# Performance work log

Hardware: AMD Instinct MI355X
Metric: run time of the kernel (lower is better)

The kernel has to match this reference:

```python
import jax, jax.numpy as jnp
import numpy as np

B, N, U, D, E = 4, 20000, 64, 1, 640000
F = U + D  # node feature dim fed to TransformerConv (state || inputs)
SCALE = 1.0 / float(np.sqrt(U))
NEG = -1e30


def setup_inputs() -> dict:
    key = jax.random.key(0)
    ks = jax.random.split(key, 20)

    def glorot(k, shape):
        s = float(np.sqrt(2.0 / (shape[0] + shape[1])))
        return jax.random.normal(k, shape, jnp.float32) * s

    inp = {
        'inputs': jax.random.normal(ks[0], (B, N), jnp.float32),
        'state': jax.random.normal(ks[1], (B, N * U), jnp.float32),
        'edge_src': jax.random.randint(ks[2], (E,), 0, N),
        'edge_dst': jax.random.randint(ks[3], (E,), 0, N),
        # TransformerConv(U+D -> U, heads=1, concat=False): query/key/value/skip linears
        'Wq': glorot(ks[4], (F, U)), 'bq': jnp.zeros((U,), jnp.float32),
        'Wk': glorot(ks[5], (F, U)), 'bk': jnp.zeros((U,), jnp.float32),
        'Wv': glorot(ks[6], (F, U)), 'bv': jnp.zeros((U,), jnp.float32),
        'Ws': glorot(ks[7], (F, U)), 'bs': jnp.zeros((U,), jnp.float32),
        # GRULinear 1: (U + D) -> 2U ; GRULinear 2: (U + D) -> U
        'W1': glorot(ks[8], (U + D, 2 * U)), 'b1': jnp.zeros((2 * U,), jnp.float32),
        'W2': glorot(ks[9], (U + D, U)), 'b2': jnp.zeros((U,), jnp.float32),
    }
    return inp


def _transformer_conv_masked(x, src, dst, Wq, bq, Wk, bk, Wv, bv, Ws, bs):
    """x: (B, N, F). PyG TransformerConv heads=1 concat=False with node/edge
    masking as in remove_nodes_and_edges (keep nodes with x[:, -7] != 0)."""
    node_mask = x[..., -7] != 0  # (B, N)
    emask = (node_mask[:, src] & node_mask[:, dst]).astype(x.dtype)  # (B, E)

    q = x @ Wq + bq  # (B, N, U)
    k = x @ Wk + bk
    v = x @ Wv + bv

    scores = jnp.einsum('beu,beu->be', q[:, dst], k[:, src]) * SCALE  # (B, E)
    scores_m = jnp.where(emask > 0, scores, NEG)
    m = jnp.full((x.shape[0], N), NEG, x.dtype).at[:, dst].max(scores_m)  # (B, N)
    e = jnp.exp(jnp.where(emask > 0, scores - m[:, dst], 0.0)) * emask  # (B, E)

    denom = jnp.zeros((x.shape[0], N), x.dtype).at[:, dst].add(e)  # (B, N)
    num = jnp.zeros((x.shape[0], N, U), x.dtype).at[:, dst].add(e[..., None] * v[:, src])
    agg = jnp.where(denom[..., None] > 0, num / jnp.maximum(denom, 1e-16)[..., None], 0.0)

    out = agg + (x @ Ws + bs)  # root/skip connection
    # nodes that were filtered out keep their original first-U feature columns (= old state)
    return jnp.where(node_mask[..., None], out, x[..., :U])  # (B, N, U)


def reference(inputs, state, edge_src, edge_dst, Wq, bq, Wk, bk, Wv, bv, Ws, bs,
              W1, b1, W2, b2):
    xin = inputs.reshape(B, N, D)
    h = state.reshape(B, N, U)
    # _gc3: TransformerConv over [state || inputs]
    x = jnp.concatenate([h, xin], axis=-1)  # (B, N, F)
    h2 = _transformer_conv_masked(x, edge_src, edge_dst, Wq, bq, Wk, bk, Wv, bv, Ws, bs)
    # GRU gates
    cat1 = jnp.concatenate([xin, h2], axis=-1)  # (B, N, U+D)
    value = jax.nn.sigmoid(cat1 @ W1 + b1)  # (B, N, 2U)
    reset, z = value[..., :U], value[..., U:]
    c = jnp.tanh(jnp.concatenate([xin, reset * h2], axis=-1) @ W2 + b2)
    new_state = (1.0 - z) * h2 + z * c
    return new_state.reshape(B, N * U)
```

## Files before the change

### kernel.cpp

```cpp
#include <hip/hip_runtime.h>
#include <hip/hip_bf16.h>

#define BB 4
#define NN 20000
#define UU 64
#define EE 640000
#define FF 65
#define SCALE_F 0.125f
#define PREP_BLOCKS 2500
#define SCAT_BLOCKS 2500

typedef unsigned short u16;
typedef unsigned long long u64;

static inline size_t align_up(size_t x) { return (x + 255) & ~(size_t)255; }

__device__ __forceinline__ float u2f(unsigned int u) { return __uint_as_float(u); }
__device__ __forceinline__ u16 f2bf(float f) {
    __hip_bfloat16 h = __float2bfloat16(f);
    return *reinterpret_cast<u16*>(&h);
}

__global__ __launch_bounds__(256) void prep_scatter_kernel(
    const float* __restrict__ state, const float* __restrict__ inputs,
    const float* __restrict__ Wk, const float* __restrict__ bk,
    const float* __restrict__ Wv, const float* __restrict__ bv,
    u16* __restrict__ kbuf, u16* __restrict__ vbuf,
    unsigned char* __restrict__ maskb,
    const int* __restrict__ edst, const int* __restrict__ esrc,
    int* __restrict__ counts, u16* __restrict__ bins, int cap) {
    int role = blockIdx.x & 1;
    int sub  = blockIdx.x >> 1;
    if (role) {
        int e = sub * 256 + threadIdx.x;
        if (e < EE) {
            int d = edst[e], s = esrc[e];
            if ((unsigned)d < (unsigned)NN && (unsigned)s < (unsigned)NN) {
                int pos = atomicAdd(&counts[d], 1);
                if (pos < cap) bins[d * cap + pos] = (u16)s;
            }
        }
        return;
    }
    int w = threadIdx.x >> 6, lane = threadIdx.x & 63;
    int gb = (sub * 4 + w) * 8;
    __shared__ float xs[4][8][66];
#pragma unroll
    for (int j = 0; j < 8; ++j) {
        int g = gb + j;
        xs[w][j][lane] = state[(size_t)g * UU + lane];
        if (lane == 0) xs[w][j][64] = inputs[g];
    }
    __syncthreads();

    float ak[8], av[8];
#pragma unroll
    for (int j = 0; j < 8; ++j) { ak[j] = 0.f; av[j] = 0.f; }
    for (int f = 0; f < FF; ++f) {
        float wk = Wk[f * UU + lane], wv = Wv[f * UU + lane];
#pragma unroll
        for (int j = 0; j < 8; ++j) {
            float xv = xs[w][j][f];
            ak[j] += xv * wk; av[j] += xv * wv;
        }
    }
    float bkl = bk[lane], bvl = bv[lane];
#pragma unroll
    for (int j = 0; j < 8; ++j) {
        int g = gb + j;
        kbuf[(size_t)g * UU + lane] = f2bf(ak[j] + bkl);
        vbuf[(size_t)g * UU + lane] = f2bf(av[j] + bvl);
        if (lane == 0) maskb[g] = (xs[w][j][58] != 0.0f) ? 1 : 0;
    }
}

__global__ __launch_bounds__(256) void fused_fast(
    const float* __restrict__ state, const float* __restrict__ inputs,
    const float* __restrict__ Wq, const float* __restrict__ bq,
    const float* __restrict__ Ws, const float* __restrict__ bs,
    const float* __restrict__ W1, const float* __restrict__ b1,
    const float* __restrict__ W2, const float* __restrict__ b2,
    const u16* __restrict__ kbuf, const u16* __restrict__ vbuf,
    const unsigned char* __restrict__ maskb,
    const int* __restrict__ counts, const u16* __restrict__ bins, int cap,
    float* __restrict__ out) {
    int w = threadIdx.x >> 6, lane = threadIdx.x & 63;
    int hl = lane & 31, hf = lane >> 5;

    int bid = blockIdx.x;
    int xcd = bid & 7;
    int b   = xcd >> 1;
    int ib  = ((bid >> 3) << 1) | (xcd & 1);
    int gb  = b * NN + ib * 16 + w * 4;

    __shared__ float xs[4][4][66];
    __shared__ float qs[4][4][68];
    __shared__ u64   pl[4][64];

#pragma unroll
    for (int j = 0; j < 4; ++j) {
        int g = gb + j;
        xs[w][j][lane] = state[(size_t)g * UU + lane];
        if (lane == 0) xs[w][j][64] = inputs[g];
    }
    __syncthreads();

    float aq[4], as_[4];
#pragma unroll
    for (int j = 0; j < 4; ++j) { aq[j] = 0.f; as_[j] = 0.f; }
    for (int f = 0; f < FF; ++f) {
        float wq = Wq[f * UU + lane], ws = Ws[f * UU + lane];
#pragma unroll
        for (int j = 0; j < 4; ++j) {
            float xv = xs[w][j][f];
            aq[j] += xv * wq; as_[j] += xv * ws;
        }
    }
    float bql = bq[lane], bsl = bs[lane];
#pragma unroll
    for (int j = 0; j < 4; ++j) {
        as_[j] += bsl;
        qs[w][j][lane] = (aq[j] + bql) * SCALE_F;
    }
    __syncthreads();

    bool mg[4];
#pragma unroll
    for (int j = 0; j < 4; ++j) mg[j] = (xs[w][j][58] != 0.0f);

    const unsigned char* mb = maskb + (size_t)b * NN;
    const u16* kb = kbuf + (size_t)b * NN * UU;
    const u16* vb = vbuf + (size_t)b * NN * UU;
    int nb = gb - b * NN;

    int cum[5]; cum[0] = 0;
    int ebase[4];
#pragma unroll
    for (int j = 0; j < 4; ++j) {
        int dg = counts[nb + j];
        dg = min(max(dg, 0), cap);
        if (!mg[j]) dg = 0;
        cum[j + 1] = cum[j] + dg;
        ebase[j] = (nb + j) * cap - cum[j];
    }
    int total = cum[4];

    float acE[4], acO[4], l[4];
#pragma unroll
    for (int j = 0; j < 4; ++j) { acE[j] = 0.f; acO[j] = 0.f; l[j] = 0.f; }

    const unsigned* vbw = (const unsigned*)vb;

#pragma unroll 1
    for (int tbase = 0; tbase < total; tbase += 64) {
        int i = tbase + lane;
        float p = 0.f; int srow = 0;
        if (i < total) {
            int jl = (i >= cum[1]) + (i >= cum[2]) + (i >= cum[3]);
            int s = bins[ebase[jl] + i];
            if (mb[s]) {
                srow = s;
                const uint4* kp = (const uint4*)(kb + ((size_t)s << 6));
                const float* qrow = &qs[w][0][0] + jl * 68;
                float d0 = 0.f, d1 = 0.f, d2 = 0.f, d3 = 0.f;
#pragma unroll
                for (int c = 0; c < 8; ++c) {
                    uint4 kk = kp[c];
                    const float4 qa = *(const float4*)&qrow[c * 8];
                    const float4 qc = *(const float4*)&qrow[c * 8 + 4];
                    d0 += u2f(kk.x << 16) * qa.x; d1 += u2f(kk.x & 0xFFFF0000u) * qa.y;
                    d2 += u2f(kk.y << 16) * qa.z; d3 += u2f(kk.y & 0xFFFF0000u) * qa.w;
                    d0 += u2f(kk.z << 16) * qc.x; d1 += u2f(kk.z & 0xFFFF0000u) * qc.y;
                    d2 += u2f(kk.w << 16) * qc.z; d3 += u2f(kk.w & 0xFFFF0000u) * qc.w;
                }
                float sc = (d0 + d1) + (d2 + d3);
                p = __expf(sc);
            }
        }
        pl[w][lane] = ((u64)(unsigned)srow << 32) | (u64)__float_as_uint(p);
        __builtin_amdgcn_wave_barrier();

#pragma unroll
        for (int j = 0; j < 4; ++j) {
            int lo = max(cum[j], tbase);
            int hi = min(cum[j + 1], tbase + 64);
#pragma unroll 1
            for (int s0 = lo; s0 < hi; s0 += 8) {
#pragma unroll
                for (int k2 = 0; k2 < 4; ++k2) {
                    int ss = s0 + 2 * k2 + hf;
                    int sidx = min(ss, hi - 1) - tbase;
                    u64 pk = pl[w][sidx];
                    float pj = (ss < hi) ? u2f((unsigned)pk) : 0.f;
                    unsigned sj = (unsigned)(pk >> 32);
                    unsigned v2 = vbw[(sj << 5) | (unsigned)hl];
                    acE[j] += pj * u2f(v2 << 16);
                    acO[j] += pj * u2f(v2 & 0xFFFF0000u);
                    l[j]   += pj;
                }
            }
        }
        __builtin_amdgcn_wave_barrier();
    }

#pragma unroll
    for (int j = 0; j < 4; ++j) {
        float lj = l[j]   + __shfl_xor(l[j],   32, 64);
        float aE = acE[j] + __shfl_xor(acE[j], 32, 64);
        float aO = acO[j] + __shfl_xor(acO[j], 32, 64);
        float vE = __shfl(aE, lane >> 1, 64);
        float vO = __shfl(aO, lane >> 1, 64);
        float acc = (lane & 1) ? vO : vE;
        float agg = (lj > 0.f) ? acc / fmaxf(lj, 1e-16f) : 0.f;
        float h2 = mg[j] ? (agg + as_[j]) : xs[w][j][lane];
        xs[w][j][lane] = h2;
    }
    __syncthreads();

    float xin[4];
#pragma unroll
    for (int j = 0; j < 4; ++j) xin[j] = xs[w][j][64];
    float a1v[4], a2v[4];
#pragma unroll
    for (int j = 0; j < 4; ++j) { a1v[j] = xin[j] * W1[lane]; a2v[j] = xin[j] * W1[UU + lane]; }
    for (int f = 0; f < UU; ++f) {
        float w1a = W1[(f + 1) * 128 + lane], w1b = W1[(f + 1) * 128 + UU + lane];
#pragma unroll
        for (int j = 0; j < 4; ++j) {
            float hv = xs[w][j][f];
            a1v[j] += hv * w1a; a2v[j] += hv * w1b;
        }
    }
    float b1a = b1[lane], b1b = b1[UU + lane];
    float rst[4], z[4];
#pragma unroll
    for (int j = 0; j < 4; ++j) {
        rst[j] = 1.f / (1.f + __expf(-(a1v[j] + b1a)));
        z[j]   = 1.f / (1.f + __expf(-(a2v[j] + b1b)));
        qs[w][j][lane] = rst[j] * xs[w][j][lane];
    }
    __syncthreads();

    float a3v[4];
#pragma unroll
    for (int j = 0; j < 4; ++j) a3v[j] = xin[j] * W2[lane];
    for (int f = 0; f < UU; ++f) {
        float w2v = W2[(f + 1) * UU + lane];
#pragma unroll
        for (int j = 0; j < 4; ++j) a3v[j] += qs[w][j][f] * w2v;
    }
    float b2l = b2[lane];
#pragma unroll
    for (int j = 0; j < 4; ++j) {
        float a = a3v[j] + b2l;
        float aa = fabsf(a), tt = __expf(-2.f * aa);
        float c = copysignf((1.f - tt) / (1.f + tt), a);
        float h2v_ = xs[w][j][lane];
        out[(size_t)(gb + j) * UU + lane] = (1.f - z[j]) * h2v_ + z[j] * c;
    }
}

extern "C" void kernel_launch(void* const* d_in, const int* in_sizes, int n_in,
                              void* d_out, int out_size, void* d_ws, size_t ws_size,
                              hipStream_t stream) {
    const float* inputs = (const float*)d_in[0];
    const float* state  = (const float*)d_in[1];
    if (in_sizes[0] != BB * NN) { inputs = (const float*)d_in[1]; state = (const float*)d_in[0]; }
    const int*   esrc   = (const int*)d_in[2];
    const int*   edst   = (const int*)d_in[3];
    const float* Wq = (const float*)d_in[4];
    const float* bq = (const float*)d_in[5];
    const float* Wk = (const float*)d_in[6];
    const float* bk = (const float*)d_in[7];
    const float* Wv = (const float*)d_in[8];
    const float* bv = (const float*)d_in[9];
    const float* Ws = (const float*)d_in[10];
    const float* bs = (const float*)d_in[11];
    const float* W1 = (const float*)d_in[12];
    const float* b1 = (const float*)d_in[13];
    const float* W2 = (const float*)d_in[14];
    const float* b2 = (const float*)d_in[15];
    float* out = (float*)d_out;

    char* base = (char*)d_ws;
    size_t ofs = 0;
    int* counts = (int*)(base + ofs); ofs = align_up(ofs + (size_t)NN * 4);
    unsigned char* maskb = (unsigned char*)(base + ofs); ofs = align_up(ofs + (size_t)BB * NN);
    u16* kbuf = (u16*)(base + ofs); ofs = align_up(ofs + (size_t)BB * NN * UU * 2);
    u16* vbuf = (u16*)(base + ofs); ofs = align_up(ofs + (size_t)BB * NN * UU * 2);
    u16* bins = (u16*)(base + ofs);
    size_t avail = (ws_size > ofs) ? (ws_size - ofs) : 0;
    int cap = (int)(avail / ((size_t)NN * 2));
    if (cap > 128) cap = 128;
    if (cap < 64)  cap = 64;
    (void)n_in; (void)out_size;

    hipMemsetAsync(counts, 0, (size_t)NN * 4, stream);
    prep_scatter_kernel<<<PREP_BLOCKS + SCAT_BLOCKS, 256, 0, stream>>>(
        state, inputs, Wk, bk, Wv, bv, kbuf, vbuf, maskb,
        edst, esrc, counts, bins, cap);
    fused_fast<<<(BB * NN) / 16, 256, 0, stream>>>(state, inputs, Wq, bq,
                                                   Ws, bs, W1, b1, W2, b2,
                                                   kbuf, vbuf, maskb,
                                                   counts, bins, cap, out);
}
```

Measured before the change: 336.9 us.

## Software-pipeline key-row gathers and bin index loads across edge chunks

Restructures the per-destination edge loop so that the key rows for the next 64-edge chunk are gathered into registers while the current chunk's value accumulation runs, and the bin indices for the chunk after that are prefetched one step earlier still. Scoring now always uses the prefetched keys and masks with a select instead of branching on the source mask, so masked edges still load keys (from row 0 or the real row). This aims to hide gather latency behind useful work, at the cost of many more live registers (16 uint4s) and possible occupancy loss.

```diff
diff --git a/kernel.cpp b/kernel.cpp
--- a/kernel.cpp
+++ b/kernel.cpp
@@ -151,34 +151,87 @@
 
     const unsigned* vbw = (const unsigned*)vb;
 
+    int sC = 0, jlC = 0; bool vC = (lane < total);
+    if (vC) { jlC = (lane >= cum[1]) + (lane >= cum[2]) + (lane >= cum[3]);
+              sC = bins[ebase[jlC] + lane]; }
+    unsigned char mC = mb[sC];
+    const uint4* kpC = (const uint4*)(kb + ((size_t)sC << 6));
+    uint4 k0 = kpC[0], k1 = kpC[1], k2 = kpC[2], k3 = kpC[3],
+          k4 = kpC[4], k5 = kpC[5], k6 = kpC[6], k7 = kpC[7];
+    int sN = 0, jlN = 0; bool vN = (64 + lane < total);
+    if (vN) { int i1 = 64 + lane;
+              jlN = (i1 >= cum[1]) + (i1 >= cum[2]) + (i1 >= cum[3]);
+              sN = bins[ebase[jlN] + i1]; }
+
 #pragma unroll 1
     for (int tbase = 0; tbase < total; tbase += 64) {
-        int i = tbase + lane;
-        float p = 0.f; int srow = 0;
-        if (i < total) {
-            int jl = (i >= cum[1]) + (i >= cum[2]) + (i >= cum[3]);
-            int s = bins[ebase[jl] + i];
-            if (mb[s]) {
-                srow = s;
-                const uint4* kp = (const uint4*)(kb + ((size_t)s << 6));
-                const float* qrow = &qs[w][0][0] + jl * 68;
-                float d0 = 0.f, d1 = 0.f, d2 = 0.f, d3 = 0.f;
-#pragma unroll
-                for (int c = 0; c < 8; ++c) {
-                    uint4 kk = kp[c];
-                    const float4 qa = *(const float4*)&qrow[c * 8];
-                    const float4 qc = *(const float4*)&qrow[c * 8 + 4];
-                    d0 += u2f(kk.x << 16) * qa.x; d1 += u2f(kk.x & 0xFFFF0000u) * qa.y;
-                    d2 += u2f(kk.y << 16) * qa.z; d3 += u2f(kk.y & 0xFFFF0000u) * qa.w;
-                    d0 += u2f(kk.z << 16) * qc.x; d1 += u2f(kk.z & 0xFFFF0000u) * qc.y;
-                    d2 += u2f(kk.w << 16) * qc.z; d3 += u2f(kk.w & 0xFFFF0000u) * qc.w;
-                }
-                float sc = (d0 + d1) + (d2 + d3);
-                p = __expf(sc);
-            }
-        }
-        pl[w][lane] = ((u64)(unsigned)srow << 32) | (u64)__float_as_uint(p);
+        int i2 = tbase + 128 + lane;
+        bool v2 = (i2 < total);
+        int jl2 = 0, s2 = 0;
+        if (v2) { jl2 = (i2 >= cum[1]) + (i2 >= cum[2]) + (i2 >= cum[3]);
+                  s2 = bins[ebase[jl2] + i2]; }
+
+        {
+            const float* qrow = &qs[w][0][0] + jlC * 68;
+            float d0 = 0.f, d1 = 0.f, d2 = 0.f, d3 = 0.f;
+            const float4 qa0 = *(const float4*)&qrow[0];
+            const float4 qb0 = *(const float4*)&qrow[4];
+            d0 += u2f(k0.x << 16) * qa0.x; d1 += u2f(k0.x & 0xFFFF0000u) * qa0.y;
+            d2 += u2f(k0.y << 16) * qa0.z; d3 += u2f(k0.y & 0xFFFF0000u) * qa0.w;
+            d0 += u2f(k0.z << 16) * qb0.x; d1 += u2f(k0.z & 0xFFFF0000u) * qb0.y;
+            d2 += u2f(k0.w << 16) * qb0.z; d3 += u2f(k0.w & 0xFFFF0000u) * qb0.w;
+            const float4 qa1 = *(const float4*)&qrow[8];
+            const float4 qb1 = *(const float4*)&qrow[12];
+            d0 += u2f(k1.x << 16) * qa1.x; d1 += u2f(k1.x & 0xFFFF0000u) * qa1.y;
+            d2 += u2f(k1.y << 16) * qa1.z; d3 += u2f(k1.y & 0xFFFF0000u) * qa1.w;
+            d0 += u2f(k1.z << 16) * qb1.x; d1 += u2f(k1.z & 0xFFFF0000u) * qb1.y;
+            d2 += u2f(k1.w << 16) * qb1.z; d3 += u2f(k1.w & 0xFFFF0000u) * qb1.w;
+            const float4 qa2 = *(const float4*)&qrow[16];
+            const float4 qb2 = *(const float4*)&qrow[20];
+            d0 += u2f(k2.x << 16) * qa2.x; d1 += u2f(k2.x & 0xFFFF0000u) * qa2.y;
+            d2 += u2f(k2.y << 16) * qa2.z; d3 += u2f(k2.y & 0xFFFF0000u) * qa2.w;
+            d0 += u2f(k2.z << 16) * qb2.x; d1 += u2f(k2.z & 0xFFFF0000u) * qb2.y;
+            d2 += u2f(k2.w << 16) * qb2.z; d3 += u2f(k2.w & 0xFFFF0000u) * qb2.w;
+            const float4 qa3 = *(const float4*)&qrow[24];
+            const float4 qb3 = *(const float4*)&qrow[28];
+            d0 += u2f(k3.x << 16) * qa3.x; d1 += u2f(k3.x & 0xFFFF0000u) * qa3.y;
+            d2 += u2f(k3.y << 16) * qa3.z; d3 += u2f(k3.y & 0xFFFF0000u) * qa3.w;
+            d0 += u2f(k3.z << 16) * qb3.x; d1 += u2f(k3.z & 0xFFFF0000u) * qb3.y;
+            d2 += u2f(k3.w << 16) * qb3.z; d3 += u2f(k3.w & 0xFFFF0000u) * qb3.w;
+            const float4 qa4 = *(const float4*)&qrow[32];
+            const float4 qb4 = *(const float4*)&qrow[36];
+            d0 += u2f(k4.x << 16) * qa4.x; d1 += u2f(k4.x & 0xFFFF0000u) * qa4.y;
+            d2 += u2f(k4.y << 16) * qa4.z; d3 += u2f(k4.y & 0xFFFF0000u) * qa4.w;
+            d0 += u2f(k4.z << 16) * qb4.x; d1 += u2f(k4.z & 0xFFFF0000u) * qb4.y;
+            d2 += u2f(k4.w << 16) * qb4.z; d3 += u2f(k4.w & 0xFFFF0000u) * qb4.w;
+            const float4 qa5 = *(const float4*)&qrow[40];
+            const float4 qb5 = *(const float4*)&qrow[44];
+            d0 += u2f(k5.x << 16) * qa5.x; d1 += u2f(k5.x & 0xFFFF0000u) * qa5.y;
+            d2 += u2f(k5.y << 16) * qa5.z; d3 += u2f(k5.y & 0xFFFF0000u) * qa5.w;
+            d0 += u2f(k5.z << 16) * qb5.x; d1 += u2f(k5.z & 0xFFFF0000u) * qb5.y;
+            d2 += u2f(k5.w << 16) * qb5.z; d3 += u2f(k5.w & 0xFFFF0000u) * qb5.w;
+            const float4 qa6 = *(const float4*)&qrow[48];
+            const float4 qb6 = *(const float4*)&qrow[52];
+            d0 += u2f(k6.x << 16) * qa6.x; d1 += u2f(k6.x & 0xFFFF0000u) * qa6.y;
+            d2 += u2f(k6.y << 16) * qa6.z; d3 += u2f(k6.y & 0xFFFF0000u) * qa6.w;
+            d0 += u2f(k6.z << 16) * qb6.x; d1 += u2f(k6.z & 0xFFFF0000u) * qb6.y;
+            d2 += u2f(k6.w << 16) * qb6.z; d3 += u2f(k6.w & 0xFFFF0000u) * qb6.w;
+            const float4 qa7 = *(const float4*)&qrow[56];
+            const float4 qb7 = *(const float4*)&qrow[60];
+            d0 += u2f(k7.x << 16) * qa7.x; d1 += u2f(k7.x & 0xFFFF0000u) * qa7.y;
+            d2 += u2f(k7.y << 16) * qa7.z; d3 += u2f(k7.y & 0xFFFF0000u) * qa7.w;
+            d0 += u2f(k7.z << 16) * qb7.x; d1 += u2f(k7.z & 0xFFFF0000u) * qb7.y;
+            d2 += u2f(k7.w << 16) * qb7.z; d3 += u2f(k7.w & 0xFFFF0000u) * qb7.w;
+            float sc = (d0 + d1) + (d2 + d3);
+            float p = (vC && mC) ? __expf(sc) : 0.f;
+            pl[w][lane] = ((u64)(unsigned)sC << 32) | (u64)__float_as_uint(p);
+        }
         __builtin_amdgcn_wave_barrier();
+
+        const uint4* kpN = (const uint4*)(kb + ((size_t)sN << 6));
+        uint4 n0 = kpN[0], n1 = kpN[1], n2 = kpN[2], n3 = kpN[3],
+              n4 = kpN[4], n5 = kpN[5], n6 = kpN[6], n7 = kpN[7];
+        unsigned char mN = mb[sN];
 
 #pragma unroll
         for (int j = 0; j < 4; ++j) {
@@ -187,20 +240,25 @@
 #pragma unroll 1
             for (int s0 = lo; s0 < hi; s0 += 8) {
 #pragma unroll
-                for (int k2 = 0; k2 < 4; ++k2) {
-                    int ss = s0 + 2 * k2 + hf;
+                for (int k2_ = 0; k2_ < 4; ++k2_) {
+                    int ss = s0 + 2 * k2_ + hf;
                     int sidx = min(ss, hi - 1) - tbase;
                     u64 pk = pl[w][sidx];
                     float pj = (ss < hi) ? u2f((unsigned)pk) : 0.f;
                     unsigned sj = (unsigned)(pk >> 32);
-                    unsigned v2 = vbw[(sj << 5) | (unsigned)hl];
-                    acE[j] += pj * u2f(v2 << 16);
-                    acO[j] += pj * u2f(v2 & 0xFFFF0000u);
+                    unsigned v2v = vbw[(sj << 5) | (unsigned)hl];
+                    acE[j] += pj * u2f(v2v << 16);
+                    acO[j] += pj * u2f(v2v & 0xFFFF0000u);
                     l[j]   += pj;
                 }
             }
         }
         __builtin_amdgcn_wave_barrier();
+
+        k0 = n0; k1 = n1; k2 = n2; k3 = n3;
+        k4 = n4; k5 = n5; k6 = n6; k7 = n7;
+        mC = mN; vC = vN; jlC = jlN; sC = sN;
+        sN = s2; jlN = jl2; vN = v2;
     }
 
 #pragma unroll
```

Measured after the change: 370.4 us. 9.9% more time.
